# Kernel optimization log

Measured on AMD Instinct MI355X. Metric: run time of the kernel, lower is better.

## Reference

```python
import jax, jax.numpy as jnp
import numpy as np


def setup_inputs() -> dict:
    key = jax.random.key(0)
    k1, k2 = jax.random.split(key)
    N, D, E = 16384, 4096, 64  # tokens, n_embd, n_exp
    x = jax.random.normal(k1, (N, D), dtype=jnp.float32)
    W = jax.random.normal(k2, (E, D), dtype=jnp.float32) * 0.02  # w_gate weight [n_exp, n_embd]
    return {"x": x, "W": W, "top_k": 4, "n_groups": 8, "n_limited_groups": 4}


def reference(x, W, top_k, n_groups, n_limited_groups):
    ROUTE_SCALE = 1.0
    N = x.shape[0]
    E = W.shape[0]
    exp_per_group = E // n_groups

    logits = x @ W.T                      # [N, E] gate linear (bias=False)
    scores = jax.nn.softmax(logits, -1)   # func == 'softmax'

    # group-limited routing: pick top n_limited_groups groups by max score (bias=False path)
    gs = scores.reshape(N, n_groups, exp_per_group)
    group_scores = gs.max(axis=-1)                             # [N, G]
    _, top_grp = jax.lax.top_k(group_scores, n_limited_groups)  # [N, L]
    selected = jnp.any(
        jnp.arange(n_groups)[None, None, :] == top_grp[:, :, None], axis=1
    )                                                           # [N, G] bool
    masked = jnp.where(selected[:, :, None], gs, -jnp.inf).reshape(N, E)

    # top-k experts over unmasked scores; weights are the gathered scores
    topk_vals, topk_idx = jax.lax.top_k(masked, top_k)          # [N, K]
    weights = (topk_vals * ROUTE_SCALE).astype(x.dtype)         # softmax -> no renorm

    # histc over expert ids
    counts = jnp.zeros((E,), jnp.int32).at[topk_idx.reshape(-1)].add(1)
    return weights, topk_idx, counts
```

## Files before the change

### kernel.cpp

```cpp
#include <hip/hip_runtime.h>
#include <math.h>

#define NTOK 16384
#define DDIM 4096
#define NEXP 64
#define KTOP 4

#define SPLITK 16
#define KPER 256
#define TPB 64
#define NBLK ((NTOK / TPB) * SPLITK)
#define WP_HL 262144

typedef __attribute__((ext_vector_type(8))) short short8;
typedef __attribute__((ext_vector_type(4))) float f32x4;


__device__ __forceinline__ unsigned short f2bf_rtn(float x) {
    unsigned int b = __float_as_uint(x);
    return (unsigned short)((b + 0x7FFFu + ((b >> 16) & 1u)) >> 16);
}
__device__ __forceinline__ float bf2f(unsigned short h) {
    return __uint_as_float(((unsigned int)h) << 16);
}
__device__ __forceinline__ void gl2lds16(const void* g, void* l) {
    __builtin_amdgcn_global_load_lds(
        (const __attribute__((address_space(1))) unsigned int*)g,
        (__attribute__((address_space(3))) unsigned int*)l, 16, 0, 0);
}
__device__ __forceinline__ unsigned int pack_hi(unsigned int u0, unsigned int u1) {
    return __builtin_amdgcn_perm(u1, u0, 0x07060302u);
}

__global__ __launch_bounds__(256) void prep_kernel(
    const float* __restrict__ W, unsigned short* __restrict__ Wp,
    float* __restrict__ counts)
{
    int idx = blockIdx.x * 256 + threadIdx.x;
    int e = idx >> 12, d = idx & 4095;
    float x = W[idx];
    unsigned short h = f2bf_rtn(x);
    float lo = x - bf2f(h);
    int s = d >> 8, p = (d >> 3) & 31, i = d & 7;
    size_t o = (((size_t)s * 32 + p) * 64 + e) * 8 + i;
    Wp[o]         = h;
    Wp[WP_HL + o] = f2bf_rtn(lo);
    if (blockIdx.x == 0 && threadIdx.x < NEXP) counts[threadIdx.x] = 0.0f;
}

__global__ __launch_bounds__(512, 4) void gemm_kernel(
    const float* __restrict__ X, const unsigned short* __restrict__ Wp,
    float* __restrict__ part)
{
    __shared__ float sX[TPB * KPER];

    const int tid  = threadIdx.x;
    const int lane = tid & 63;
    const int w    = tid >> 6;
    const int qm   = w >> 2;
    const int qn   = w & 3;
    const int tb   = blockIdx.x >> 4;
    const int s    = blockIdx.x & 15;
    const int kbase = s * KPER;
    const int tok0 = tb * TPB;

    #pragma unroll
    for (int i = 0; i < 8; ++i) {
        const int r = w * 8 + i;
        const float* src = X + (size_t)(tok0 + r) * DDIM + kbase
                         + ((lane ^ (r & 7)) << 2);
        gl2lds16(src, &sX[r * KPER]);
    }

    const int fr = lane & 15;
    const int fg = lane >> 4;
    const size_t e8 = (size_t)(qn * 16 + fr) * 8;
    short8 bh[8], bl[8];
    #pragma unroll
    for (int ks = 0; ks < 8; ++ks) {
        const size_t o = ((size_t)(s * 32 + ks * 4 + fg)) * 512 + e8;
        bh[ks] = *(const short8*)(Wp + o);
        bl[ks] = *(const short8*)(Wp + WP_HL + o);
    }

    __syncthreads();

    const int key = fr & 7;
    int baseA[2][2];
    #pragma unroll
    for (int mg = 0; mg < 2; ++mg) {
        const int row = qm * 32 + mg * 16 + fr;
        baseA[mg][0] = row * KPER + (((fg * 2    ) ^ key) << 2);
        baseA[mg][1] = row * KPER + (((fg * 2 + 1) ^ key) << 2);
    }

    f32x4 acc[2];
    acc[0] = (f32x4){0.f, 0.f, 0.f, 0.f};
    acc[1] = (f32x4){0.f, 0.f, 0.f, 0.f};

    #pragma unroll
    for (int ks = 0; ks < 8; ++ks) {
        #pragma unroll
        for (int mg = 0; mg < 2; ++mg) {
            const float4 qa = *(const float4*)&sX[baseA[mg][0] + ks * 32];
            const float4 qb = *(const float4*)&sX[baseA[mg][1] + ks * 32];

            const unsigned int u0 = __float_as_uint(qa.x), u1 = __float_as_uint(qa.y);
            const unsigned int u2 = __float_as_uint(qa.z), u3 = __float_as_uint(qa.w);
            const unsigned int u4 = __float_as_uint(qb.x), u5 = __float_as_uint(qb.y);
            const unsigned int u6 = __float_as_uint(qb.z), u7 = __float_as_uint(qb.w);
            union { unsigned int u[4]; short8 s8; } ah, al;
            ah.u[0] = pack_hi(u0, u1);
            ah.u[1] = pack_hi(u2, u3);
            ah.u[2] = pack_hi(u4, u5);
            ah.u[3] = pack_hi(u6, u7);
            const float l0 = qa.x - __uint_as_float(u0 & 0xFFFF0000u);
            const float l1 = qa.y - __uint_as_float(u1 & 0xFFFF0000u);
            const float l2 = qa.z - __uint_as_float(u2 & 0xFFFF0000u);
            const float l3 = qa.w - __uint_as_float(u3 & 0xFFFF0000u);
            const float l4 = qb.x - __uint_as_float(u4 & 0xFFFF0000u);
            const float l5 = qb.y - __uint_as_float(u5 & 0xFFFF0000u);
            const float l6 = qb.z - __uint_as_float(u6 & 0xFFFF0000u);
            const float l7 = qb.w - __uint_as_float(u7 & 0xFFFF0000u);
            al.u[0] = pack_hi(__float_as_uint(l0), __float_as_uint(l1));
            al.u[1] = pack_hi(__float_as_uint(l2), __float_as_uint(l3));
            al.u[2] = pack_hi(__float_as_uint(l4), __float_as_uint(l5));
            al.u[3] = pack_hi(__float_as_uint(l6), __float_as_uint(l7));

            acc[mg] = __builtin_amdgcn_mfma_f32_16x16x32_bf16(ah.s8, bh[ks], acc[mg], 0, 0, 0);
            acc[mg] = __builtin_amdgcn_mfma_f32_16x16x32_bf16(ah.s8, bl[ks], acc[mg], 0, 0, 0);
            acc[mg] = __builtin_amdgcn_mfma_f32_16x16x32_bf16(al.s8, bh[ks], acc[mg], 0, 0, 0);
        }
    }

    #pragma unroll
    for (int mg = 0; mg < 2; ++mg)
        #pragma unroll
        for (int r = 0; r < 4; ++r) {
            const int n = tok0 + qm * 32 + mg * 16 + fg * 4 + r;
            part[((size_t)n * SPLITK + s) * NEXP + qn * 16 + fr] = acc[mg][r];
        }
}

__global__ __launch_bounds__(256) void route_kernel(
    const float* __restrict__ part, float* __restrict__ outW,
    float* __restrict__ outI, float* __restrict__ counts)
{
    __shared__ int hist[NEXP];
    const int tid = threadIdx.x;
    if (tid < NEXP) hist[tid] = 0;
    __syncthreads();

    const int lane = tid & 63;
    const int wv   = tid >> 6;
    const int tok_base = blockIdx.x * 32 + wv * 8;

    for (int t = 0; t < 8; ++t) {
        const int n = tok_base + t;
        float L = 0.0f;
        #pragma unroll
        for (int s = 0; s < SPLITK; ++s)
            L += part[((size_t)n * SPLITK + s) * NEXP + lane];

        float m = L;
        #pragma unroll
        for (int off = 32; off > 0; off >>= 1) m = fmaxf(m, __shfl_xor(m, off));
        float p = expf(L - m);
        float ssum = p;
        #pragma unroll
        for (int off = 32; off > 0; off >>= 1) ssum += __shfl_xor(ssum, off);
        const float score = p / ssum;

        float gm = score;
        gm = fmaxf(gm, __shfl_xor(gm, 1));
        gm = fmaxf(gm, __shfl_xor(gm, 2));
        gm = fmaxf(gm, __shfl_xor(gm, 4));

        float ga[8];
        #pragma unroll
        for (int g = 0; g < 8; ++g) ga[g] = __shfl(gm, g * 8);
        unsigned selmask = 0u;
        #pragma unroll
        for (int r = 0; r < 4; ++r) {
            float best = -INFINITY; int bg = 0;
            #pragma unroll
            for (int g = 0; g < 8; ++g) {
                bool taken  = (selmask >> g) & 1u;
                bool better = (!taken) && (ga[g] > best);
                bg   = better ? g : bg;
                best = better ? ga[g] : best;
            }
            selmask |= (1u << bg);
        }

        float ms = ((selmask >> (lane >> 3)) & 1u) ? score : -INFINITY;
        float wk[4]; int wi[4];
        #pragma unroll
        for (int r = 0; r < 4; ++r) {
            float v = ms; int ix = lane;
            #pragma unroll
            for (int off = 32; off > 0; off >>= 1) {
                float vo = __shfl_xor(v, off);
                int   io = __shfl_xor(ix, off);
                if (vo > v || (vo == v && io < ix)) { v = vo; ix = io; }
            }
            wk[r] = v; wi[r] = ix;
            if (lane == ix) ms = -INFINITY;
        }

        if (lane == 0) {
            *(float4*)&outW[(size_t)n * 4] = make_float4(wk[0], wk[1], wk[2], wk[3]);
            *(float4*)&outI[(size_t)n * 4] =
                make_float4((float)wi[0], (float)wi[1], (float)wi[2], (float)wi[3]);
            atomicAdd(&hist[wi[0]], 1);
            atomicAdd(&hist[wi[1]], 1);
            atomicAdd(&hist[wi[2]], 1);
            atomicAdd(&hist[wi[3]], 1);
        }
    }

    __syncthreads();
    if (tid < NEXP) atomicAdd(&counts[tid], (float)hist[tid]);
}

extern "C" void kernel_launch(void* const* d_in, const int* in_sizes, int n_in,
                              void* d_out, int out_size, void* d_ws, size_t ws_size,
                              hipStream_t stream) {
    const float* X = (const float*)d_in[0];
    const float* W = (const float*)d_in[1];

    float* outW   = (float*)d_out;
    float* outI   = outW + (size_t)NTOK * KTOP;
    float* counts = outW + (size_t)2 * NTOK * KTOP;

    float*          part = (float*)d_ws;
    unsigned short* Wp   = (unsigned short*)(part + (size_t)NTOK * SPLITK * NEXP);

    prep_kernel<<<(NEXP * DDIM) / 256, 256, 0, stream>>>(W, Wp, counts);
    gemm_kernel<<<NBLK, 512, 0, stream>>>(X, Wp, part);
    route_kernel<<<NTOK / 32, 256, 0, stream>>>(part, outW, outI, counts);
}
```

Baseline: 119.8 us.

## Double-buffer X tiles in LDS and cut split-K from sixteen to four

```diff
diff --git a/kernel.cpp b/kernel.cpp
--- a/kernel.cpp
+++ b/kernel.cpp
@@ -6,8 +6,10 @@
 #define NEXP 64
 #define KTOP 4
 
-#define SPLITK 16
-#define KPER 256
+#define SPLITK 4
+#define KPER (DDIM / SPLITK)
+#define BK 128
+#define NSTG (KPER / BK)
 #define TPB 64
 #define NBLK ((NTOK / TPB) * SPLITK)
 #define WP_HL 262144
@@ -41,8 +43,7 @@
     float x = W[idx];
     unsigned short h = f2bf_rtn(x);
     float lo = x - bf2f(h);
-    int s = d >> 8, p = (d >> 3) & 31, i = d & 7;
-    size_t o = (((size_t)s * 32 + p) * 64 + e) * 8 + i;
+    size_t o = (((size_t)(d >> 3)) * 64 + e) * 8 + (d & 7);
     Wp[o]         = h;
     Wp[WP_HL + o] = f2bf_rtn(lo);
     if (blockIdx.x == 0 && threadIdx.x < NEXP) counts[threadIdx.x] = 0.0f;
@@ -52,86 +53,105 @@
     const float* __restrict__ X, const unsigned short* __restrict__ Wp,
     float* __restrict__ part)
 {
-    __shared__ float sX[TPB * KPER];
+    __shared__ float sX[2][TPB * BK];
 
     const int tid  = threadIdx.x;
     const int lane = tid & 63;
     const int w    = tid >> 6;
     const int qm   = w >> 2;
     const int qn   = w & 3;
-    const int tb   = blockIdx.x >> 4;
-    const int s    = blockIdx.x & 15;
+    const int tb   = blockIdx.x >> 2;
+    const int s    = blockIdx.x & 3;
     const int kbase = s * KPER;
     const int tok0 = tb * TPB;
 
+    const float* xsrc[4];
+    int xdst[4];
     #pragma unroll
-    for (int i = 0; i < 8; ++i) {
-        const int r = w * 8 + i;
-        const float* src = X + (size_t)(tok0 + r) * DDIM + kbase
-                         + ((lane ^ (r & 7)) << 2);
-        gl2lds16(src, &sX[r * KPER]);
-    }
-
-    const int fr = lane & 15;
-    const int fg = lane >> 4;
-    const size_t e8 = (size_t)(qn * 16 + fr) * 8;
-    short8 bh[8], bl[8];
-    #pragma unroll
-    for (int ks = 0; ks < 8; ++ks) {
-        const size_t o = ((size_t)(s * 32 + ks * 4 + fg)) * 512 + e8;
-        bh[ks] = *(const short8*)(Wp + o);
-        bl[ks] = *(const short8*)(Wp + WP_HL + o);
-    }
-
+    for (int i = 0; i < 4; ++i) {
+        const int r = w * 8 + i * 2 + (lane >> 5);
+        const int p = lane & 31;
+        xsrc[i] = X + (size_t)(tok0 + r) * DDIM + kbase + ((p ^ (r & 7)) << 2);
+        xdst[i] = (w * 8 + i * 2) * BK;
+    }
+
+#define XISSUE(st_, buf_)                                                   \
+    {                                                                       \
+        _Pragma("unroll")                                                   \
+        for (int i = 0; i < 4; ++i)                                         \
+            gl2lds16(xsrc[i] + (st_) * BK, &sX[buf_][xdst[i]]);             \
+    }
+
+    XISSUE(0, 0)
     __syncthreads();
 
+    const int fr  = lane & 15;
+    const int fg  = lane >> 4;
     const int key = fr & 7;
-    int baseA[2][2];
-    #pragma unroll
-    for (int mg = 0; mg < 2; ++mg) {
-        const int row = qm * 32 + mg * 16 + fr;
-        baseA[mg][0] = row * KPER + (((fg * 2    ) ^ key) << 2);
-        baseA[mg][1] = row * KPER + (((fg * 2 + 1) ^ key) << 2);
-    }
+    const int e8    = (qn * 16 + fr) * 8;
+    const int pbase = kbase >> 3;
+    int rowA[2];
+    rowA[0] = (qm * 32 + fr) * BK;
+    rowA[1] = (qm * 32 + 16 + fr) * BK;
 
     f32x4 acc[2];
     acc[0] = (f32x4){0.f, 0.f, 0.f, 0.f};
     acc[1] = (f32x4){0.f, 0.f, 0.f, 0.f};
 
     #pragma unroll
-    for (int ks = 0; ks < 8; ++ks) {
-        #pragma unroll
-        for (int mg = 0; mg < 2; ++mg) {
-            const float4 qa = *(const float4*)&sX[baseA[mg][0] + ks * 32];
-            const float4 qb = *(const float4*)&sX[baseA[mg][1] + ks * 32];
-
-            const unsigned int u0 = __float_as_uint(qa.x), u1 = __float_as_uint(qa.y);
-            const unsigned int u2 = __float_as_uint(qa.z), u3 = __float_as_uint(qa.w);
-            const unsigned int u4 = __float_as_uint(qb.x), u5 = __float_as_uint(qb.y);
-            const unsigned int u6 = __float_as_uint(qb.z), u7 = __float_as_uint(qb.w);
-            union { unsigned int u[4]; short8 s8; } ah, al;
-            ah.u[0] = pack_hi(u0, u1);
-            ah.u[1] = pack_hi(u2, u3);
-            ah.u[2] = pack_hi(u4, u5);
-            ah.u[3] = pack_hi(u6, u7);
-            const float l0 = qa.x - __uint_as_float(u0 & 0xFFFF0000u);
-            const float l1 = qa.y - __uint_as_float(u1 & 0xFFFF0000u);
-            const float l2 = qa.z - __uint_as_float(u2 & 0xFFFF0000u);
-            const float l3 = qa.w - __uint_as_float(u3 & 0xFFFF0000u);
-            const float l4 = qb.x - __uint_as_float(u4 & 0xFFFF0000u);
-            const float l5 = qb.y - __uint_as_float(u5 & 0xFFFF0000u);
-            const float l6 = qb.z - __uint_as_float(u6 & 0xFFFF0000u);
-            const float l7 = qb.w - __uint_as_float(u7 & 0xFFFF0000u);
-            al.u[0] = pack_hi(__float_as_uint(l0), __float_as_uint(l1));
-            al.u[1] = pack_hi(__float_as_uint(l2), __float_as_uint(l3));
-            al.u[2] = pack_hi(__float_as_uint(l4), __float_as_uint(l5));
-            al.u[3] = pack_hi(__float_as_uint(l6), __float_as_uint(l7));
-
-            acc[mg] = __builtin_amdgcn_mfma_f32_16x16x32_bf16(ah.s8, bh[ks], acc[mg], 0, 0, 0);
-            acc[mg] = __builtin_amdgcn_mfma_f32_16x16x32_bf16(ah.s8, bl[ks], acc[mg], 0, 0, 0);
-            acc[mg] = __builtin_amdgcn_mfma_f32_16x16x32_bf16(al.s8, bh[ks], acc[mg], 0, 0, 0);
-        }
-    }
+    for (int t = 0; t < NSTG; ++t) {
+        short8 bh[4], bl[4];
+        #pragma unroll
+        for (int ks = 0; ks < 4; ++ks) {
+            const size_t o = (size_t)(pbase + t * 16 + ks * 4 + fg) * 512 + e8;
+            bh[ks] = *(const short8*)(Wp + o);
+            bl[ks] = *(const short8*)(Wp + WP_HL + o);
+        }
+        asm volatile("" ::: "memory");
+
+        if (t + 1 < NSTG) XISSUE(t + 1, (t + 1) & 1)
+
+        const float* cx = sX[t & 1];
+        #pragma unroll
+        for (int ks = 0; ks < 4; ++ks) {
+            #pragma unroll
+            for (int mg = 0; mg < 2; ++mg) {
+                const int p0 = (ks * 8 + fg * 2) ^ key;
+                const int p1 = (ks * 8 + fg * 2 + 1) ^ key;
+                const float4 qa = *(const float4*)&cx[rowA[mg] + (p0 << 2)];
+                const float4 qb = *(const float4*)&cx[rowA[mg] + (p1 << 2)];
+
+                const unsigned int u0 = __float_as_uint(qa.x), u1 = __float_as_uint(qa.y);
+                const unsigned int u2 = __float_as_uint(qa.z), u3 = __float_as_uint(qa.w);
+                const unsigned int u4 = __float_as_uint(qb.x), u5 = __float_as_uint(qb.y);
+                const unsigned int u6 = __float_as_uint(qb.z), u7 = __float_as_uint(qb.w);
+                union { unsigned int u[4]; short8 s8; } ah, al;
+                ah.u[0] = pack_hi(u0, u1);
+                ah.u[1] = pack_hi(u2, u3);
+                ah.u[2] = pack_hi(u4, u5);
+                ah.u[3] = pack_hi(u6, u7);
+                const float l0 = qa.x - __uint_as_float(u0 & 0xFFFF0000u);
+                const float l1 = qa.y - __uint_as_float(u1 & 0xFFFF0000u);
+                const float l2 = qa.z - __uint_as_float(u2 & 0xFFFF0000u);
+                const float l3 = qa.w - __uint_as_float(u3 & 0xFFFF0000u);
+                const float l4 = qb.x - __uint_as_float(u4 & 0xFFFF0000u);
+                const float l5 = qb.y - __uint_as_float(u5 & 0xFFFF0000u);
+                const float l6 = qb.z - __uint_as_float(u6 & 0xFFFF0000u);
+                const float l7 = qb.w - __uint_as_float(u7 & 0xFFFF0000u);
+                al.u[0] = pack_hi(__float_as_uint(l0), __float_as_uint(l1));
+                al.u[1] = pack_hi(__float_as_uint(l2), __float_as_uint(l3));
+                al.u[2] = pack_hi(__float_as_uint(l4), __float_as_uint(l5));
+                al.u[3] = pack_hi(__float_as_uint(l6), __float_as_uint(l7));
+
+                acc[mg] = __builtin_amdgcn_mfma_f32_16x16x32_bf16(ah.s8, bh[ks], acc[mg], 0, 0, 0);
+                acc[mg] = __builtin_amdgcn_mfma_f32_16x16x32_bf16(ah.s8, bl[ks], acc[mg], 0, 0, 0);
+                acc[mg] = __builtin_amdgcn_mfma_f32_16x16x32_bf16(al.s8, bh[ks], acc[mg], 0, 0, 0);
+            }
+        }
+
+        __syncthreads();
+    }
+#undef XISSUE
 
     #pragma unroll
     for (int mg = 0; mg < 2; ++mg)
```

New measurement: 115.1 us. 1.04x faster.

## Warp-specialize gate GEMM with producer/consumer LDS ring pipeline and larger token tiles

Applied to the files above, without the earlier changes.

```diff
diff --git a/kernel.cpp b/kernel.cpp
--- a/kernel.cpp
+++ b/kernel.cpp
@@ -6,10 +6,14 @@
 #define NEXP 64
 #define KTOP 4
 
-#define SPLITK 16
-#define KPER 256
-#define TPB 64
+#define SPLITK 8
+#define KPER (DDIM / SPLITK)
+#define BK 32
+#define NSTG (KPER / BK)
+#define TPB 256
 #define NBLK ((NTOK / TPB) * SPLITK)
+#define NCONS 8
+#define NPROD 4
 #define WP_HL 262144
 
 typedef __attribute__((ext_vector_type(8))) short short8;
@@ -30,6 +34,11 @@
 }
 __device__ __forceinline__ unsigned int pack_hi(unsigned int u0, unsigned int u1) {
     return __builtin_amdgcn_perm(u1, u0, 0x07060302u);
+}
+__device__ __forceinline__ void poll_ge(unsigned* p, unsigned tgt) {
+    while (__hip_atomic_load(p, __ATOMIC_ACQUIRE, __HIP_MEMORY_SCOPE_WORKGROUP) < tgt)
+        __builtin_amdgcn_s_sleep(1);
+    __builtin_amdgcn_sched_barrier(0);
 }
 
 __global__ __launch_bounds__(256) void prep_kernel(
@@ -41,69 +50,105 @@
     float x = W[idx];
     unsigned short h = f2bf_rtn(x);
     float lo = x - bf2f(h);
-    int s = d >> 8, p = (d >> 3) & 31, i = d & 7;
-    size_t o = (((size_t)s * 32 + p) * 64 + e) * 8 + i;
+    size_t o = (((size_t)(d >> 3)) * 64 + e) * 8 + (d & 7);
     Wp[o]         = h;
     Wp[WP_HL + o] = f2bf_rtn(lo);
     if (blockIdx.x == 0 && threadIdx.x < NEXP) counts[threadIdx.x] = 0.0f;
 }
 
-__global__ __launch_bounds__(512, 4) void gemm_kernel(
+__global__ __launch_bounds__(768, 3) void gemm_kernel(
     const float* __restrict__ X, const unsigned short* __restrict__ Wp,
     float* __restrict__ part)
 {
-    __shared__ float sX[TPB * KPER];
+    __shared__ float ring[4][TPB * BK];
+    __shared__ unsigned rdy[4];
+    __shared__ unsigned dn[4];
 
     const int tid  = threadIdx.x;
     const int lane = tid & 63;
     const int w    = tid >> 6;
-    const int qm   = w >> 2;
-    const int qn   = w & 3;
-    const int tb   = blockIdx.x >> 4;
-    const int s    = blockIdx.x & 15;
+    const int tb   = blockIdx.x >> 3;
+    const int s    = blockIdx.x & 7;
     const int kbase = s * KPER;
     const int tok0 = tb * TPB;
 
-    #pragma unroll
-    for (int i = 0; i < 8; ++i) {
-        const int r = w * 8 + i;
-        const float* src = X + (size_t)(tok0 + r) * DDIM + kbase
-                         + ((lane ^ (r & 7)) << 2);
-        gl2lds16(src, &sX[r * KPER]);
-    }
-
+    if (tid < 4) rdy[tid] = 0;
+    else if (tid < 8) dn[tid - 4] = 0;
+    __syncthreads();
+
+    if (w >= NCONS) {
+        const int pw = w - NCONS;
+        const float* src[8];
+        int dst[8];
+        #pragma unroll
+        for (int j = 0; j < 8; ++j) {
+            const int r = pw * 64 + j * 8 + (lane >> 3);
+            src[j] = X + (size_t)(tok0 + r) * DDIM + kbase
+                   + (((lane & 7) ^ (r & 7)) << 2);
+            dst[j] = (pw * 64 + j * 8) * BK;
+        }
+        #pragma unroll 1
+        for (int st = 0; st < NSTG; ++st) {
+            const int slot = st & 3;
+            if (st >= 4) poll_ge(&dn[slot], 8u * (unsigned)(st >> 2));
+            #pragma unroll
+            for (int j = 0; j < 8; ++j)
+                gl2lds16(src[j] + st * BK, &ring[slot][dst[j]]);
+            if (st >= 1) {
+                asm volatile("s_waitcnt vmcnt(8)" ::: "memory");
+                if (lane == 0)
+                    __hip_atomic_fetch_add(&rdy[(st - 1) & 3], 1u,
+                        __ATOMIC_RELEASE, __HIP_MEMORY_SCOPE_WORKGROUP);
+            }
+        }
+        asm volatile("s_waitcnt vmcnt(0)" ::: "memory");
+        if (lane == 0)
+            __hip_atomic_fetch_add(&rdy[(NSTG - 1) & 3], 1u,
+                __ATOMIC_RELEASE, __HIP_MEMORY_SCOPE_WORKGROUP);
+        return;
+    }
+
+    const int qm = w >> 2;
+    const int qn = w & 3;
     const int fr = lane & 15;
     const int fg = lane >> 4;
-    const size_t e8 = (size_t)(qn * 16 + fr) * 8;
-    short8 bh[8], bl[8];
+    const int key = fr & 7;
+    const int e8  = (qn * 16 + fr) * 8;
+    const int pb  = kbase >> 3;
+
+    f32x4 acc[8];
     #pragma unroll
-    for (int ks = 0; ks < 8; ++ks) {
-        const size_t o = ((size_t)(s * 32 + ks * 4 + fg)) * 512 + e8;
-        bh[ks] = *(const short8*)(Wp + o);
-        bl[ks] = *(const short8*)(Wp + WP_HL + o);
-    }
-
-    __syncthreads();
-
-    const int key = fr & 7;
-    int baseA[2][2];
+    for (int mg = 0; mg < 8; ++mg) acc[mg] = (f32x4){0.f, 0.f, 0.f, 0.f};
+
+    short8 bh0, bl0, bh1, bl1;
+    {
+        const size_t o = (size_t)(pb + 0 * 4 + fg) * 512 + e8;
+        bh0 = *(const short8*)(Wp + o);
+        bl0 = *(const short8*)(Wp + WP_HL + o);
+    }
+
     #pragma unroll
-    for (int mg = 0; mg < 2; ++mg) {
-        const int row = qm * 32 + mg * 16 + fr;
-        baseA[mg][0] = row * KPER + (((fg * 2    ) ^ key) << 2);
-        baseA[mg][1] = row * KPER + (((fg * 2 + 1) ^ key) << 2);
-    }
-
-    f32x4 acc[2];
-    acc[0] = (f32x4){0.f, 0.f, 0.f, 0.f};
-    acc[1] = (f32x4){0.f, 0.f, 0.f, 0.f};
-
-    #pragma unroll
-    for (int ks = 0; ks < 8; ++ks) {
-        #pragma unroll
-        for (int mg = 0; mg < 2; ++mg) {
-            const float4 qa = *(const float4*)&sX[baseA[mg][0] + ks * 32];
-            const float4 qb = *(const float4*)&sX[baseA[mg][1] + ks * 32];
+    for (int st = 0; st < NSTG; ++st) {
+        const int slot = st & 3;
+        poll_ge(&rdy[slot], 4u * (unsigned)((st >> 2) + 1));
+
+        if (st + 1 < NSTG) {
+            const size_t o = (size_t)(pb + (st + 1) * 4 + fg) * 512 + e8;
+            if ((st & 1) == 0) { bh1 = *(const short8*)(Wp + o);
+                                 bl1 = *(const short8*)(Wp + WP_HL + o); }
+            else               { bh0 = *(const short8*)(Wp + o);
+                                 bl0 = *(const short8*)(Wp + WP_HL + o); }
+        }
+        const short8 bh = (st & 1) ? bh1 : bh0;
+        const short8 bl = (st & 1) ? bl1 : bl0;
+
+        const float* cx = ring[slot];
+        #pragma unroll
+        for (int mg = 0; mg < 8; ++mg) {
+            const int lr = qm * 128 + mg * 16 + fr;
+            const int p0 = (fg * 2) ^ key;
+            const float4 qa = *(const float4*)&cx[lr * BK + (p0 << 2)];
+            const float4 qb = *(const float4*)&cx[lr * BK + ((p0 ^ 1) << 2)];
 
             const unsigned int u0 = __float_as_uint(qa.x), u1 = __float_as_uint(qa.y);
             const unsigned int u2 = __float_as_uint(qa.z), u3 = __float_as_uint(qa.w);
@@ -127,17 +172,21 @@
             al.u[2] = pack_hi(__float_as_uint(l4), __float_as_uint(l5));
             al.u[3] = pack_hi(__float_as_uint(l6), __float_as_uint(l7));
 
-            acc[mg] = __builtin_amdgcn_mfma_f32_16x16x32_bf16(ah.s8, bh[ks], acc[mg], 0, 0, 0);
-            acc[mg] = __builtin_amdgcn_mfma_f32_16x16x32_bf16(ah.s8, bl[ks], acc[mg], 0, 0, 0);
-            acc[mg] = __builtin_amdgcn_mfma_f32_16x16x32_bf16(al.s8, bh[ks], acc[mg], 0, 0, 0);
-        }
+            acc[mg] = __builtin_amdgcn_mfma_f32_16x16x32_bf16(ah.s8, bh, acc[mg], 0, 0, 0);
+            acc[mg] = __builtin_amdgcn_mfma_f32_16x16x32_bf16(ah.s8, bl, acc[mg], 0, 0, 0);
+            acc[mg] = __builtin_amdgcn_mfma_f32_16x16x32_bf16(al.s8, bh, acc[mg], 0, 0, 0);
+        }
+
+        if (lane == 0)
+            __hip_atomic_fetch_add(&dn[slot], 1u,
+                __ATOMIC_RELEASE, __HIP_MEMORY_SCOPE_WORKGROUP);
     }
 
     #pragma unroll
-    for (int mg = 0; mg < 2; ++mg)
+    for (int mg = 0; mg < 8; ++mg)
         #pragma unroll
         for (int r = 0; r < 4; ++r) {
-            const int n = tok0 + qm * 32 + mg * 16 + fg * 4 + r;
+            const int n = tok0 + qm * 128 + mg * 16 + fg * 4 + r;
             part[((size_t)n * SPLITK + s) * NEXP + qn * 16 + fr] = acc[mg][r];
         }
 }
@@ -237,6 +286,6 @@
     unsigned short* Wp   = (unsigned short*)(part + (size_t)NTOK * SPLITK * NEXP);
 
     prep_kernel<<<(NEXP * DDIM) / 256, 256, 0, stream>>>(W, Wp, counts);
-    gemm_kernel<<<NBLK, 512, 0, stream>>>(X, Wp, part);
+    gemm_kernel<<<NBLK, (NCONS + NPROD) * 64, 0, stream>>>(X, Wp, part);
     route_kernel<<<NTOK / 32, 256, 0, stream>>>(part, outW, outI, counts);
 }
```

After: 104.7 us. 1.14x faster.
